# Optimization experiments

Measured on AMD Instinct MI355X. Metric: run time of the kernel, lower is better.

## Reference

```python
import jax, jax.numpy as jnp
import numpy as np
import math

GROUPS = 32
EPS = 1e-5
N_HEADS = 8  # channels=512 / num_head_channels=64


def group_norm(x, w, b):
    # x: [B, C, T]; GroupNorm over (channels-in-group, T)
    B, C, T = x.shape
    xg = x.reshape(B, GROUPS, C // GROUPS * T)
    mu = xg.mean(axis=-1, keepdims=True)
    var = xg.var(axis=-1, keepdims=True)
    xn = ((xg - mu) * jax.lax.rsqrt(var + EPS)).reshape(B, C, T)
    return xn * w[None, :, None] + b[None, :, None]


def setup_inputs() -> dict:
    key = jax.random.key(0)
    ks = jax.random.split(key, 7)
    C = 512
    return {
        "x": jax.random.normal(ks[0], (8, C, 32, 32), dtype=jnp.float32),
        "norm_w": jax.random.normal(ks[1], (C,), dtype=jnp.float32),
        "norm_b": jax.random.normal(ks[2], (C,), dtype=jnp.float32),
        "qkv_w": jax.random.normal(ks[3], (3 * C, C), dtype=jnp.float32) * 0.02,
        "qkv_b": jax.random.normal(ks[4], (3 * C,), dtype=jnp.float32) * 0.02,
        "proj_w": jax.random.normal(ks[5], (C, C), dtype=jnp.float32) * 0.02,
        "proj_b": jax.random.normal(ks[6], (C,), dtype=jnp.float32) * 0.02,
    }


def reference(x, norm_w, norm_b, qkv_w, qkv_b, proj_w, proj_b):
    b, c, H, W = x.shape
    T = H * W
    xf = x.reshape(b, c, T)
    xn = group_norm(xf, norm_w, norm_b)
    # 1x1 conv1d == channel matmul: [3C, C] x [B, C, T] -> [B, 3C, T]
    qkv = jnp.einsum('oc,bct->bot', qkv_w, xn) + qkv_b[None, :, None]
    ch = c // N_HEADS
    qkv = qkv.reshape(b * N_HEADS, 3 * ch, T)
    q, k, v = qkv[:, :ch], qkv[:, ch:2 * ch], qkv[:, 2 * ch:]
    scale = 1.0 / math.sqrt(math.sqrt(ch))
    # [BH, T, T] score matrix (explicit, as in the original)
    weight = jnp.einsum('bct,bcs->bts', q * scale, k * scale)
    weight = jax.nn.softmax(weight.astype(jnp.float32), axis=-1).astype(qkv.dtype)
    a = jnp.einsum('bts,bcs->bct', weight, v).reshape(b, c, T)
    hout = jnp.einsum('oc,bct->bot', proj_w, a) + proj_b[None, :, None]
    return (xf + hout).reshape(b, c, H, W)
```

## Files before the change

kernel.cpp:

```cpp
#include <hip/hip_runtime.h>
#include <math.h>

typedef float f32x4_t __attribute__((ext_vector_type(4)));
typedef short bf16x8_t __attribute__((ext_vector_type(8)));

#define B_   8
#define C_   512
#define T_   1024
#define NH_  8
#define CH_  64
#define EPSF 1e-5f

#define MFMA16(a, b, c) __builtin_amdgcn_mfma_f32_16x16x32_bf16((a), (b), (c), 0, 0, 0)

__device__ __forceinline__ unsigned short f2bf(float f) {
  union { float f; unsigned u; } v; v.f = f;
  unsigned r = v.u + 0x7FFFu + ((v.u >> 16) & 1u);
  return (unsigned short)(r >> 16);
}

__global__ __launch_bounds__(256) void prep_gn_kernel(
    const float* __restrict__ x, const float* __restrict__ w,
    const float* __restrict__ bvec, unsigned short* __restrict__ xnT,
    const float* __restrict__ qw_f, const float* __restrict__ pw_f,
    unsigned short* __restrict__ qw, unsigned short* __restrict__ pw)
{
  int tid = threadIdx.x;
  if (blockIdx.x >= 256) {
    int idx = (blockIdx.x - 256) * 256 + tid;
    const int N1 = 1536 * 512 / 4;
    const int N2 = 512 * 512 / 4;
    if (idx < N1) {
      float4 v = ((const float4*)qw_f)[idx];
      uint2 o;
      o.x = (unsigned)f2bf(v.x) | ((unsigned)f2bf(v.y) << 16);
      o.y = (unsigned)f2bf(v.z) | ((unsigned)f2bf(v.w) << 16);
      ((uint2*)qw)[idx] = o;
    } else if (idx < N1 + N2) {
      int j = idx - N1;
      float4 v = ((const float4*)pw_f)[j];
      uint2 o;
      o.x = (unsigned)f2bf(v.x) | ((unsigned)f2bf(v.y) << 16);
      o.y = (unsigned)f2bf(v.z) | ((unsigned)f2bf(v.w) << 16);
      ((uint2*)pw)[j] = o;
    }
    return;
  }

  int blk = blockIdx.x;
  int b = blk >> 5, g = blk & 31;
  const float* xp = x + ((size_t)(b * C_ + g * 16)) * T_;
  const int N = 16 * T_;

  float s = 0.f, s2 = 0.f;
  for (int i = tid * 4; i < N; i += 256 * 4) {
    float4 v = *(const float4*)(xp + i);
    s  += v.x + v.y + v.z + v.w;
    s2 += v.x * v.x + v.y * v.y + v.z * v.z + v.w * v.w;
  }
  for (int off = 32; off; off >>= 1) {
    s  += __shfl_down(s,  off, 64);
    s2 += __shfl_down(s2, off, 64);
  }
  __shared__ float rs_[4], r2_[4];
  __shared__ float mu_s, rsig_s;
  int wid = tid >> 6, lane = tid & 63;
  if (lane == 0) { rs_[wid] = s; r2_[wid] = s2; }
  __syncthreads();
  if (tid == 0) {
    float ts = rs_[0] + rs_[1] + rs_[2] + rs_[3];
    float t2 = r2_[0] + r2_[1] + r2_[2] + r2_[3];
    float mu = ts / (float)N;
    float var = t2 / (float)N - mu * mu;
    mu_s = mu;
    rsig_s = rsqrtf(var + EPSF);
  }
  __syncthreads();
  float mu = mu_s, rs = rsig_s;

  float wl[16], bl[16];
  for (int c = 0; c < 16; ++c) { wl[c] = w[g * 16 + c]; bl[c] = bvec[g * 16 + c]; }

  for (int t = tid; t < T_; t += 256) {
    unsigned short buf[16] __attribute__((aligned(16)));
    for (int c = 0; c < 16; ++c) {
      float val = xp[(size_t)c * T_ + t];
      buf[c] = f2bf((val - mu) * rs * wl[c] + bl[c]);
    }
    unsigned short* dst = xnT + ((size_t)b * T_ + t) * C_ + g * 16;
    *(uint4*)dst       = *(uint4*)buf;
    *(uint4*)(dst + 8) = *(uint4*)(buf + 8);
  }
}

__global__ __launch_bounds__(256) void gemm_qkv_kernel(
    const unsigned short* __restrict__ W, const unsigned short* __restrict__ xnT,
    const float* __restrict__ bias,
    unsigned short* __restrict__ q_t, unsigned short* __restrict__ k_t,
    unsigned short* __restrict__ v_c)
{
  int b = blockIdx.z;
  int m0 = blockIdx.y * 128, n0 = blockIdx.x * 128;
  int tid = threadIdx.x;
  int w = tid >> 6, lane = tid & 63, quad = lane >> 4, lr = lane & 15;
  int wm = w >> 1, wn = w & 1;

  __shared__ __align__(16) unsigned short Asl[128][40];
  __shared__ __align__(16) unsigned short Bsl[128][40];

  f32x4_t acc[4][4];
  for (int i = 0; i < 4; ++i)
    for (int j = 0; j < 4; ++j) acc[i][j] = (f32x4_t){0.f, 0.f, 0.f, 0.f};

  const unsigned short* Bbase = xnT + ((size_t)b * T_ + n0) * C_;

  int ur = tid >> 2, uk = (tid & 3) * 8;
  uint4 pa0 = *(const uint4*)&W[(size_t)(m0 + ur) * C_ + uk];
  uint4 pa1 = *(const uint4*)&W[(size_t)(m0 + ur + 64) * C_ + uk];
  uint4 pb0 = *(const uint4*)&Bbase[(size_t)ur * C_ + uk];
  uint4 pb1 = *(const uint4*)&Bbase[(size_t)(ur + 64) * C_ + uk];

  for (int k0 = 0; k0 < C_; k0 += 32) {
    __syncthreads();
    *(uint4*)&Asl[ur][uk]      = pa0;
    *(uint4*)&Asl[ur + 64][uk] = pa1;
    *(uint4*)&Bsl[ur][uk]      = pb0;
    *(uint4*)&Bsl[ur + 64][uk] = pb1;
    if (k0 + 32 < C_) {
      pa0 = *(const uint4*)&W[(size_t)(m0 + ur) * C_ + k0 + 32 + uk];
      pa1 = *(const uint4*)&W[(size_t)(m0 + ur + 64) * C_ + k0 + 32 + uk];
      pb0 = *(const uint4*)&Bbase[(size_t)ur * C_ + k0 + 32 + uk];
      pb1 = *(const uint4*)&Bbase[(size_t)(ur + 64) * C_ + k0 + 32 + uk];
    }
    __syncthreads();
    bf16x8_t af[4], bfv[4];
    for (int i = 0; i < 4; ++i) af[i]  = *(bf16x8_t*)&Asl[wm * 64 + i * 16 + lr][quad * 8];
    for (int j = 0; j < 4; ++j) bfv[j] = *(bf16x8_t*)&Bsl[wn * 64 + j * 16 + lr][quad * 8];
    for (int i = 0; i < 4; ++i)
      for (int j = 0; j < 4; ++j)
        acc[i][j] = MFMA16(af[i], bfv[j], acc[i][j]);
  }

  for (int i = 0; i < 4; ++i) {
    int ob = m0 + wm * 64 + i * 16 + quad * 4;
    int h = ob / 192, r0 = ob % 192;
    for (int j = 0; j < 4; ++j) {
      int t = n0 + wn * 64 + j * 16 + lr;
      if (r0 < 128) {
        unsigned short pk[4] __attribute__((aligned(8)));
      #pragma unroll
        for (int r = 0; r < 4; ++r) pk[r] = f2bf(acc[i][j][r] + bias[ob + r]);
        unsigned short* base = (r0 < 64) ? q_t : k_t;
        int chn = (r0 < 64) ? r0 : r0 - 64;
        *(uint2*)&base[((size_t)(b * NH_ + h) * T_ + t) * CH_ + chn] = *(uint2*)pk;
      } else {
      #pragma unroll
        for (int r = 0; r < 4; ++r) {
          float vv = acc[i][j][r] + bias[ob + r];
          v_c[((size_t)(b * NH_ + h) * CH_ + (r0 - 128 + r)) * T_ + t] = f2bf(vv);
        }
      }
    }
  }
}

__global__ __launch_bounds__(256) void attn_kernel(
    const unsigned short* __restrict__ q_t, const unsigned short* __restrict__ k_t,
    const unsigned short* __restrict__ v_c, unsigned short* __restrict__ a_t)
{
  int bh = blockIdx.x;
  int t0 = blockIdx.y * 64;
  int tid = threadIdx.x;
  int w = tid >> 6, lane = tid & 63, quad = lane >> 4, lr = lane & 15;

  __shared__ __align__(16) unsigned short q_s[64][72];
  __shared__ __align__(16) unsigned short k_s[64][72];
  __shared__ __align__(16) unsigned short v_s[64][72];
  __shared__ __align__(16) unsigned short p_s[64][72];

  int r0 = tid >> 3, c0 = (tid & 7) * 8;
  *(uint4*)&q_s[r0][c0] =
      *(const uint4*)&q_t[((size_t)bh * T_ + t0 + r0) * CH_ + c0];
  *(uint4*)&q_s[r0 + 32][c0] =
      *(const uint4*)&q_t[((size_t)bh * T_ + t0 + r0 + 32) * CH_ + c0];

  uint4 kr0 = *(const uint4*)&k_t[((size_t)bh * T_ + r0) * CH_ + c0];
  uint4 kr1 = *(const uint4*)&k_t[((size_t)bh * T_ + r0 + 32) * CH_ + c0];
  uint4 vr0 = *(const uint4*)&v_c[((size_t)bh * CH_ + r0) * T_ + c0];
  uint4 vr1 = *(const uint4*)&v_c[((size_t)bh * CH_ + r0 + 32) * T_ + c0];

  __syncthreads();
  bf16x8_t aq[2];
  aq[0] = *(bf16x8_t*)&q_s[w * 16 + lr][quad * 8];
  aq[1] = *(bf16x8_t*)&q_s[w * 16 + lr][32 + quad * 8];

  bf16x8_t ones8;
  {
    short ov = (lr == 0) ? (short)0x3F80 : (short)0;
    for (int e = 0; e < 8; ++e) ones8[e] = ov;
  }

  f32x4_t o_acc[4], o_l;
  for (int j = 0; j < 4; ++j) o_acc[j] = (f32x4_t){0.f, 0.f, 0.f, 0.f};
  o_l = (f32x4_t){0.f, 0.f, 0.f, 0.f};

  const float SCL = 0.18033688f;
  const float MSH = 11.541560f;

  for (int s0 = 0; s0 < T_; s0 += 64) {
    __syncthreads();
    *(uint4*)&k_s[r0][c0]      = kr0;
    *(uint4*)&k_s[r0 + 32][c0] = kr1;
    *(uint4*)&v_s[r0][c0]      = vr0;
    *(uint4*)&v_s[r0 + 32][c0] = vr1;
    if (s0 + 64 < T_) {
      kr0 = *(const uint4*)&k_t[((size_t)bh * T_ + s0 + 64 + r0) * CH_ + c0];
      kr1 = *(const uint4*)&k_t[((size_t)bh * T_ + s0 + 96 + r0) * CH_ + c0];
      vr0 = *(const uint4*)&v_c[((size_t)bh * CH_ + r0) * T_ + s0 + 64 + c0];
      vr1 = *(const uint4*)&v_c[((size_t)bh * CH_ + r0 + 32) * T_ + s0 + 64 + c0];
    }
    __syncthreads();

    f32x4_t sc[4];
    for (int j = 0; j < 4; ++j) {
      f32x4_t a2 = (f32x4_t){0.f, 0.f, 0.f, 0.f};
      for (int kk = 0; kk < 2; ++kk) {
        bf16x8_t bk = *(bf16x8_t*)&k_s[j * 16 + lr][kk * 32 + quad * 8];
        a2 = MFMA16(aq[kk], bk, a2);
      }
      sc[j] = a2;
    }

    for (int j = 0; j < 4; ++j)
      for (int r = 0; r < 4; ++r) {
        float p = __builtin_amdgcn_exp2f(sc[j][r] * SCL - MSH);
        union { float f; unsigned u; } cv; cv.f = p;
        p_s[w * 16 + quad * 4 + r][j * 16 + lr] = (unsigned short)(cv.u >> 16);
      }
    bf16x8_t ap[2];
    ap[0] = *(bf16x8_t*)&p_s[w * 16 + lr][quad * 8];
    ap[1] = *(bf16x8_t*)&p_s[w * 16 + lr][32 + quad * 8];

    o_l = MFMA16(ap[0], ones8, o_l);
    o_l = MFMA16(ap[1], ones8, o_l);
    for (int j = 0; j < 4; ++j)
      for (int kk = 0; kk < 2; ++kk) {
        bf16x8_t bv = *(bf16x8_t*)&v_s[j * 16 + lr][kk * 32 + quad * 8];
        o_acc[j] = MFMA16(ap[kk], bv, o_acc[j]);
      }
  }

  float lv[4];
  for (int r = 0; r < 4; ++r) lv[r] = __shfl(o_l[r], lane & 48, 64);
  for (int r = 0; r < 4; ++r) {
    float inv = 1.f / lv[r];
    for (int j = 0; j < 4; ++j)
      q_s[w * 16 + quad * 4 + r][j * 16 + lr] = f2bf(o_acc[j][r] * inv);
  }
  __syncthreads();
  *(uint4*)&a_t[((size_t)bh * T_ + t0 + r0) * CH_ + c0]      = *(uint4*)&q_s[r0][c0];
  *(uint4*)&a_t[((size_t)bh * T_ + t0 + r0 + 32) * CH_ + c0] = *(uint4*)&q_s[r0 + 32][c0];
}

__global__ __launch_bounds__(256) void gemm_proj_kernel(
    const unsigned short* __restrict__ W, const unsigned short* __restrict__ a_t,
    const float* __restrict__ bias, const float* __restrict__ xres,
    float* __restrict__ out)
{
  int b = blockIdx.z;
  int m0 = blockIdx.y * 128, n0 = blockIdx.x * 128;
  int tid = threadIdx.x;
  int w = tid >> 6, lane = tid & 63, quad = lane >> 4, lr = lane & 15;
  int wm = w >> 1, wn = w & 1;

  __shared__ __align__(16) unsigned short Asl[128][40];
  __shared__ __align__(16) unsigned short Bsl[128][40];

  f32x4_t acc[4][4];
  for (int i = 0; i < 4; ++i)
    for (int j = 0; j < 4; ++j) acc[i][j] = (f32x4_t){0.f, 0.f, 0.f, 0.f};

  int ur = tid >> 2, uk = (tid & 3) * 8;
  const unsigned short* Bb0 = a_t + ((size_t)(b * NH_ + 0) * T_ + n0) * CH_;
  uint4 pa0 = *(const uint4*)&W[(size_t)(m0 + ur) * C_ + uk];
  uint4 pa1 = *(const uint4*)&W[(size_t)(m0 + ur + 64) * C_ + uk];
  uint4 pb0 = *(const uint4*)&Bb0[(size_t)ur * CH_ + uk];
  uint4 pb1 = *(const uint4*)&Bb0[(size_t)(ur + 64) * CH_ + uk];

  for (int k0 = 0; k0 < C_; k0 += 32) {
    __syncthreads();
    *(uint4*)&Asl[ur][uk]      = pa0;
    *(uint4*)&Asl[ur + 64][uk] = pa1;
    *(uint4*)&Bsl[ur][uk]      = pb0;
    *(uint4*)&Bsl[ur + 64][uk] = pb1;
    if (k0 + 32 < C_) {
      int kn = k0 + 32;
      const unsigned short* Bb =
          a_t + ((size_t)(b * NH_ + (kn >> 6)) * T_ + n0) * CH_ + (kn & 63);
      pa0 = *(const uint4*)&W[(size_t)(m0 + ur) * C_ + kn + uk];
      pa1 = *(const uint4*)&W[(size_t)(m0 + ur + 64) * C_ + kn + uk];
      pb0 = *(const uint4*)&Bb[(size_t)ur * CH_ + uk];
      pb1 = *(const uint4*)&Bb[(size_t)(ur + 64) * CH_ + uk];
    }
    __syncthreads();
    bf16x8_t af[4], bfv[4];
    for (int i = 0; i < 4; ++i) af[i]  = *(bf16x8_t*)&Asl[wm * 64 + i * 16 + lr][quad * 8];
    for (int j = 0; j < 4; ++j) bfv[j] = *(bf16x8_t*)&Bsl[wn * 64 + j * 16 + lr][quad * 8];
    for (int i = 0; i < 4; ++i)
      for (int j = 0; j < 4; ++j)
        acc[i][j] = MFMA16(af[i], bfv[j], acc[i][j]);
  }

  for (int i = 0; i < 4; ++i) {
    int ob = m0 + wm * 64 + i * 16 + quad * 4;
    for (int j = 0; j < 4; ++j) {
      int t = n0 + wn * 64 + j * 16 + lr;
    #pragma unroll
      for (int r = 0; r < 4; ++r) {
        size_t idx = ((size_t)(b * C_ + ob + r)) * T_ + t;
        out[idx] = acc[i][j][r] + bias[ob + r] + xres[idx];
      }
    }
  }
}

extern "C" void kernel_launch(void* const* d_in, const int* in_sizes, int n_in,
                              void* d_out, int out_size, void* d_ws, size_t ws_size,
                              hipStream_t stream)
{
  const float* x      = (const float*)d_in[0];
  const float* norm_w = (const float*)d_in[1];
  const float* norm_b = (const float*)d_in[2];
  const float* qkv_w  = (const float*)d_in[3];
  const float* qkv_b  = (const float*)d_in[4];
  const float* proj_w = (const float*)d_in[5];
  const float* proj_b = (const float*)d_in[6];
  float* out = (float*)d_out;

  char* ws = (char*)d_ws;
  unsigned short* qw  = (unsigned short*)ws;
  unsigned short* pw  = (unsigned short*)(ws + 1572864);
  unsigned short* xnT = (unsigned short*)(ws + 2097152);
  unsigned short* q_t = (unsigned short*)(ws + 10485760);
  unsigned short* k_t = (unsigned short*)(ws + 18874368);
  unsigned short* v_c = (unsigned short*)(ws + 27262976);
  unsigned short* a_t = (unsigned short*)(ws + 35651584);

  prep_gn_kernel<<<dim3(256 + 1024), dim3(256), 0, stream>>>(
      x, norm_w, norm_b, xnT, qkv_w, proj_w, qw, pw);

  gemm_qkv_kernel<<<dim3(T_ / 128, 1536 / 128, B_), dim3(256), 0, stream>>>(
      qw, xnT, qkv_b, q_t, k_t, v_c);

  attn_kernel<<<dim3(B_ * NH_, T_ / 64), dim3(256), 0, stream>>>(q_t, k_t, v_c, a_t);

  gemm_proj_kernel<<<dim3(T_ / 128, C_ / 128, B_), dim3(256), 0, stream>>>(
      pw, a_t, proj_b, x, out);
}
```

Before: 167.9 us.

## Use direct global-to-LDS loads with double-buffered shared tiles in QKV and proj GEMMs

Both GEMM kernels now stage A and B tiles with global_load_lds, which writes straight into shared memory and skips the register round-trip. Two shared buffers let the next k-slice load while MFMAs run on the current one, cutting one barrier per iteration. The unpadded [128][32] layout can cause LDS bank conflicts on the fragment reads, and correctness relies on the barrier ordering the async LDS writes.

```diff
diff --git a/kernel.cpp b/kernel.cpp
--- a/kernel.cpp
+++ b/kernel.cpp
@@ -12,6 +12,10 @@
 #define EPSF 1e-5f
 
 #define MFMA16(a, b, c) __builtin_amdgcn_mfma_f32_16x16x32_bf16((a), (b), (c), 0, 0, 0)
+
+#define GLD16(gp, lp) __builtin_amdgcn_global_load_lds( \
+    (const __attribute__((address_space(1))) unsigned int*)(gp), \
+    (__attribute__((address_space(3))) unsigned int*)(lp), 16, 0, 0)
 
 __device__ __forceinline__ unsigned short f2bf(float f) {
   union { float f; unsigned u; } v; v.f = f;
@@ -105,41 +109,41 @@
   int w = tid >> 6, lane = tid & 63, quad = lane >> 4, lr = lane & 15;
   int wm = w >> 1, wn = w & 1;
 
-  __shared__ __align__(16) unsigned short Asl[128][40];
-  __shared__ __align__(16) unsigned short Bsl[128][40];
+  __shared__ __align__(16) unsigned short Asl[2][128][32];
+  __shared__ __align__(16) unsigned short Bsl[2][128][32];
 
   f32x4_t acc[4][4];
   for (int i = 0; i < 4; ++i)
     for (int j = 0; j < 4; ++j) acc[i][j] = (f32x4_t){0.f, 0.f, 0.f, 0.f};
 
-  const unsigned short* Bbase = xnT + ((size_t)b * T_ + n0) * C_;
-
   int ur = tid >> 2, uk = (tid & 3) * 8;
-  uint4 pa0 = *(const uint4*)&W[(size_t)(m0 + ur) * C_ + uk];
-  uint4 pa1 = *(const uint4*)&W[(size_t)(m0 + ur + 64) * C_ + uk];
-  uint4 pb0 = *(const uint4*)&Bbase[(size_t)ur * C_ + uk];
-  uint4 pb1 = *(const uint4*)&Bbase[(size_t)(ur + 64) * C_ + uk];
-
+  const unsigned short* Ap = W + (size_t)(m0 + ur) * C_ + uk;
+  const unsigned short* Bp = xnT + ((size_t)b * T_ + n0 + ur) * C_ + uk;
+
+#define STAGE_QKV(buf, k0)                                        \
+  do {                                                            \
+    GLD16(Ap + (k0),            &Asl[buf][w * 16][0]);            \
+    GLD16(Ap + 64 * C_ + (k0),  &Asl[buf][64 + w * 16][0]);       \
+    GLD16(Bp + (k0),            &Bsl[buf][w * 16][0]);            \
+    GLD16(Bp + 64 * C_ + (k0),  &Bsl[buf][64 + w * 16][0]);       \
+  } while (0)
+
+  STAGE_QKV(0, 0);
+  __syncthreads();
+
+  int cur = 0;
   for (int k0 = 0; k0 < C_; k0 += 32) {
-    __syncthreads();
-    *(uint4*)&Asl[ur][uk]      = pa0;
-    *(uint4*)&Asl[ur + 64][uk] = pa1;
-    *(uint4*)&Bsl[ur][uk]      = pb0;
-    *(uint4*)&Bsl[ur + 64][uk] = pb1;
-    if (k0 + 32 < C_) {
-      pa0 = *(const uint4*)&W[(size_t)(m0 + ur) * C_ + k0 + 32 + uk];
-      pa1 = *(const uint4*)&W[(size_t)(m0 + ur + 64) * C_ + k0 + 32 + uk];
-      pb0 = *(const uint4*)&Bbase[(size_t)ur * C_ + k0 + 32 + uk];
-      pb1 = *(const uint4*)&Bbase[(size_t)(ur + 64) * C_ + k0 + 32 + uk];
-    }
-    __syncthreads();
+    if (k0 + 32 < C_) STAGE_QKV(cur ^ 1, k0 + 32);
     bf16x8_t af[4], bfv[4];
-    for (int i = 0; i < 4; ++i) af[i]  = *(bf16x8_t*)&Asl[wm * 64 + i * 16 + lr][quad * 8];
-    for (int j = 0; j < 4; ++j) bfv[j] = *(bf16x8_t*)&Bsl[wn * 64 + j * 16 + lr][quad * 8];
+    for (int i = 0; i < 4; ++i) af[i]  = *(bf16x8_t*)&Asl[cur][wm * 64 + i * 16 + lr][quad * 8];
+    for (int j = 0; j < 4; ++j) bfv[j] = *(bf16x8_t*)&Bsl[cur][wn * 64 + j * 16 + lr][quad * 8];
     for (int i = 0; i < 4; ++i)
       for (int j = 0; j < 4; ++j)
         acc[i][j] = MFMA16(af[i], bfv[j], acc[i][j]);
-  }
+    __syncthreads();
+    cur ^= 1;
+  }
+#undef STAGE_QKV
 
   for (int i = 0; i < 4; ++i) {
     int ob = m0 + wm * 64 + i * 16 + quad * 4;
@@ -273,43 +277,42 @@
   int w = tid >> 6, lane = tid & 63, quad = lane >> 4, lr = lane & 15;
   int wm = w >> 1, wn = w & 1;
 
-  __shared__ __align__(16) unsigned short Asl[128][40];
-  __shared__ __align__(16) unsigned short Bsl[128][40];
+  __shared__ __align__(16) unsigned short Asl[2][128][32];
+  __shared__ __align__(16) unsigned short Bsl[2][128][32];
 
   f32x4_t acc[4][4];
   for (int i = 0; i < 4; ++i)
     for (int j = 0; j < 4; ++j) acc[i][j] = (f32x4_t){0.f, 0.f, 0.f, 0.f};
 
   int ur = tid >> 2, uk = (tid & 3) * 8;
-  const unsigned short* Bb0 = a_t + ((size_t)(b * NH_ + 0) * T_ + n0) * CH_;
-  uint4 pa0 = *(const uint4*)&W[(size_t)(m0 + ur) * C_ + uk];
-  uint4 pa1 = *(const uint4*)&W[(size_t)(m0 + ur + 64) * C_ + uk];
-  uint4 pb0 = *(const uint4*)&Bb0[(size_t)ur * CH_ + uk];
-  uint4 pb1 = *(const uint4*)&Bb0[(size_t)(ur + 64) * CH_ + uk];
-
+  const unsigned short* Ap = W + (size_t)(m0 + ur) * C_ + uk;
+
+#define STAGE_PROJ(buf, k0)                                                   \
+  do {                                                                        \
+    const unsigned short* Bp = a_t +                                          \
+        ((size_t)(b * NH_ + ((k0) >> 6)) * T_ + n0 + ur) * CH_ + ((k0) & 63) + uk; \
+    GLD16(Ap + (k0),           &Asl[buf][w * 16][0]);                         \
+    GLD16(Ap + 64 * C_ + (k0), &Asl[buf][64 + w * 16][0]);                    \
+    GLD16(Bp,                  &Bsl[buf][w * 16][0]);                         \
+    GLD16(Bp + 64 * CH_,       &Bsl[buf][64 + w * 16][0]);                    \
+  } while (0)
+
+  STAGE_PROJ(0, 0);
+  __syncthreads();
+
+  int cur = 0;
   for (int k0 = 0; k0 < C_; k0 += 32) {
-    __syncthreads();
-    *(uint4*)&Asl[ur][uk]      = pa0;
-    *(uint4*)&Asl[ur + 64][uk] = pa1;
-    *(uint4*)&Bsl[ur][uk]      = pb0;
-    *(uint4*)&Bsl[ur + 64][uk] = pb1;
-    if (k0 + 32 < C_) {
-      int kn = k0 + 32;
-      const unsigned short* Bb =
-          a_t + ((size_t)(b * NH_ + (kn >> 6)) * T_ + n0) * CH_ + (kn & 63);
-      pa0 = *(const uint4*)&W[(size_t)(m0 + ur) * C_ + kn + uk];
-      pa1 = *(const uint4*)&W[(size_t)(m0 + ur + 64) * C_ + kn + uk];
-      pb0 = *(const uint4*)&Bb[(size_t)ur * CH_ + uk];
-      pb1 = *(const uint4*)&Bb[(size_t)(ur + 64) * CH_ + uk];
-    }
-    __syncthreads();
+    if (k0 + 32 < C_) STAGE_PROJ(cur ^ 1, k0 + 32);
     bf16x8_t af[4], bfv[4];
-    for (int i = 0; i < 4; ++i) af[i]  = *(bf16x8_t*)&Asl[wm * 64 + i * 16 + lr][quad * 8];
-    for (int j = 0; j < 4; ++j) bfv[j] = *(bf16x8_t*)&Bsl[wn * 64 + j * 16 + lr][quad * 8];
+    for (int i = 0; i < 4; ++i) af[i]  = *(bf16x8_t*)&Asl[cur][wm * 64 + i * 16 + lr][quad * 8];
+    for (int j = 0; j < 4; ++j) bfv[j] = *(bf16x8_t*)&Bsl[cur][wn * 64 + j * 16 + lr][quad * 8];
     for (int i = 0; i < 4; ++i)
       for (int j = 0; j < 4; ++j)
         acc[i][j] = MFMA16(af[i], bfv[j], acc[i][j]);
-  }
+    __syncthreads();
+    cur ^= 1;
+  }
+#undef STAGE_PROJ
 
   for (int i = 0; i < 4; ++i) {
     int ob = m0 + wm * 64 + i * 16 + quad * 4;
```

New measurement: 168.7 us. About the same (+0.5%).
